# Performance work log

Measured on AMD Instinct MI355X. Metric: run time of the kernel, lower is better.

Reference implementation:

```python
import jax, jax.numpy as jnp
import numpy as np

DIM = 128      # input node feature dim
GS = 64        # SAGEConv output dim
AF = 32        # additional (ir_score) feature dim
NB = 2         # nb_classes
G = 8192       # num_graphs in batch
NPG = 16       # nodes per graph
N = G * NPG    # total nodes = 131072
E = 2097152    # total edges (avg degree 16)


def setup_inputs() -> dict:
    key = jax.random.key(0)
    ks = jax.random.split(key, 10)

    def w(k, shape, fan_in):
        return jax.random.normal(k, shape, jnp.float32) / np.sqrt(fan_in)

    return {
        "x": jax.random.normal(ks[0], (N, DIM), jnp.float32),
        "edge_index": jax.random.randint(ks[1], (2, E), 0, N),
        "set_indices": jax.random.randint(ks[2], (G, 2), 0, NPG),
        "batch_ids": jnp.repeat(jnp.arange(G), NPG),  # sorted graph ids, PyG style
        "ir_score": jax.random.uniform(ks[3], (G, AF), jnp.float32),
        "W_l": w(ks[4], (DIM, GS), DIM),
        "b_l": jnp.zeros((GS,), jnp.float32),
        "W_r": w(ks[5], (DIM, GS), DIM),
        "W_ir": w(ks[6], (AF, 2 * GS), AF),
        "b_ir": jnp.zeros((2 * GS,), jnp.float32),
        "W1": w(ks[7], ((2 * GS) * (2 * GS), 200), (2 * GS) * (2 * GS)),
        "b1": jnp.zeros((200,), jnp.float32),
        "W2": w(ks[8], (200, NB), 200),
        "b2": jnp.zeros((NB,), jnp.float32),
    }


def reference(x, edge_index, set_indices, batch_ids, ir_score,
              W_l, b_l, W_r, W_ir, b_ir, W1, b1, W2, b2):
    n = x.shape[0]
    src, dst = edge_index[0], edge_index[1]

    # SAGEConv (mean aggregation): out = lin_l(mean_{j in N(i)} x_j) + lin_r(x_i)
    agg = jax.ops.segment_sum(x[src], dst, num_segments=n)           # [N, DIM]
    deg = jax.ops.segment_sum(jnp.ones((src.shape[0],), x.dtype), dst, num_segments=n)
    mean = agg / jnp.maximum(deg, 1.0)[:, None]
    h = jax.nn.relu(mean @ W_l + b_l + x @ W_r)                      # [N, GS]

    # per-graph node counts -> index bases (cumsum), then global pair indices
    g = set_indices.shape[0]
    num_nodes = jax.ops.segment_sum(jnp.ones((n,), jnp.float32), batch_ids, num_segments=g)
    csum = jnp.cumsum(num_nodes.astype(jnp.int64))
    index_bases = jnp.concatenate([jnp.zeros((1,), jnp.int64), csum[:-1]])
    sib = index_bases[:, None] + set_indices                         # [G, 2]

    pair = h[sib].reshape(g, 2 * GS)                                 # gather + flatten

    # fusion: relu(linear(ir_score)) then per-graph outer product
    S = jax.nn.relu(ir_score @ W_ir + b_ir)                          # [G, 2*GS]
    outer = jnp.einsum('gi,gj->gij', pair, S).reshape(g, -1)         # [G, (2GS)^2]

    # decode MLP
    z = jax.nn.relu(outer @ W1 + b1)                                 # [G, 200]
    logits = z @ W2 + b2                                             # [G, NB]
    return logits
```

## Files before the change

### kernel.cpp

```cpp
#include <hip/hip_runtime.h>

#define NN   131072
#define GG   8192
#define EE   2097152
#define KBIG 16384
#define NPAD 224
#define NSPLIT 8
#define NSEL  16384
#define SBUCK 256
#define SUBC  4
#define SCAPS 336
#define SCAPT (SUBC*SCAPS)

typedef _Float16 half_t;
typedef __attribute__((ext_vector_type(8))) _Float16 half8;
typedef __attribute__((ext_vector_type(4))) float floatx4;

__device__ inline floatx4 mfma16(half8 a, half8 b, floatx4 c) {
  return __builtin_amdgcn_mfma_f32_16x16x32_f16(a, b, c, 0, 0, 0);
}

__global__ void prep_w(const float* __restrict__ Wl, const float* __restrict__ Wr,
                       half_t* __restrict__ Wt) {
  int idx = blockIdx.x * blockDim.x + threadIdx.x;
  int n = idx >> 7, k = idx & 127;
  float v = (n < 64) ? Wl[k * 64 + n] : Wr[k * 64 + (n - 64)];
  Wt[n * 128 + k] = (half_t)v;
}
__global__ void prep_w1p(const float* __restrict__ W1, half_t* __restrict__ W1p) {
  int idx = blockIdx.x * blockDim.x + threadIdx.x;
  int lane = idx & 63;
  int t = idx >> 6;
  int nt = t % 14; t /= 14;
  int jj = t & 1;  t >>= 1;
  int i  = t & 15; t >>= 4;
  int ph = t & 1;  t >>= 1;
  int split = t;
  int n = nt * 16 + (lane & 15);
  int k0 = split * 2048 + i * 128 + ph * 64 + jj * 32 + (lane >> 4) * 8;
  half8 v;
#pragma unroll
  for (int e = 0; e < 8; e++)
    v[e] = (half_t)((n < 200) ? W1[(size_t)(k0 + e) * 200 + n] : 0.f);
  *(half8*)(W1p + (size_t)idx * 8) = v;
}

__global__ void set_slots(const int* __restrict__ set_idx, int* __restrict__ nodemap,
                          int* __restrict__ slot_node) {
  int idx = blockIdx.x * blockDim.x + threadIdx.x;
  int g = idx >> 1, which = idx & 1;
  int node = g * 16 + set_idx[g * 2 + which];
  slot_node[idx] = node;
  nodemap[node] = idx;
}

__global__ void filter_scatter(const int* __restrict__ src, const int* __restrict__ dst,
                               const int* __restrict__ nodemap,
                               int* __restrict__ scnt, unsigned int* __restrict__ sbuf) {
  int e = blockIdx.x * blockDim.x + threadIdx.x;
  int d = dst[e];
  int slot = nodemap[d];
  if (slot >= 0) {
    int b = slot >> 6;
    int sub = blockIdx.x & (SUBC - 1);
    int pos = atomicAdd(&scnt[(b * SUBC + sub) * 16], 1);
    if (pos < SCAPS)
      sbuf[(size_t)(b * SUBC + sub) * SCAPS + pos] =
          (unsigned int)src[e] | ((unsigned int)(slot & 63) << 17);
  }
}

__global__ __launch_bounds__(256) void y_gemm(const float* __restrict__ x,
                                              const half_t* __restrict__ WtG,
                                              half_t* __restrict__ y16) {
  __shared__ half_t wlds[64 * 128];
  __shared__ half_t ybuf[64 * 72];
  int tid = threadIdx.x, w = tid >> 6, lane = tid & 63;
  int m = lane & 15, q = lane >> 4, kc = q * 8;
#pragma unroll
  for (int it = 0; it < 4; it++) {
    int cb = (it * 4 + w) * 64;
    const half_t* g = WtG + ((size_t)cb + lane) * 8;
    half_t* l = wlds + (size_t)cb * 8;
    __builtin_amdgcn_global_load_lds((const __attribute__((address_space(1))) uint32_t*)g,
                                     (__attribute__((address_space(3))) uint32_t*)l, 16, 0, 0);
  }
  int node0 = blockIdx.x * 64 + w * 16;
  float4 xu[4][2];
#pragma unroll
  for (int step = 0; step < 4; step++) {
    const float* xp = x + (size_t)(node0 + m) * 128 + step * 32 + kc;
    xu[step][0] = *(const float4*)xp;
    xu[step][1] = *(const float4*)(xp + 4);
  }
  __syncthreads();
  floatx4 acc[4];
#pragma unroll
  for (int nt = 0; nt < 4; nt++) acc[nt] = (floatx4){0.f, 0.f, 0.f, 0.f};
#pragma unroll
  for (int step = 0; step < 4; step++) {
    float4 u0 = xu[step][0], u1 = xu[step][1];
    half8 av = {(half_t)u0.x, (half_t)u0.y, (half_t)u0.z, (half_t)u0.w,
                (half_t)u1.x, (half_t)u1.y, (half_t)u1.z, (half_t)u1.w};
    int k0 = step * 32 + kc;
#pragma unroll
    for (int nt = 0; nt < 4; nt++) {
      half8 bv = *(const half8*)(wlds + (nt * 16 + m) * 128 + k0);
      acc[nt] = mfma16(av, bv, acc[nt]);
    }
  }
#pragma unroll
  for (int nt = 0; nt < 4; nt++)
#pragma unroll
    for (int r = 0; r < 4; r++)
      ybuf[(w * 16 + q * 4 + r) * 72 + nt * 16 + m] = (half_t)acc[nt][r];
  __syncthreads();
#pragma unroll
  for (int c = tid; c < 512; c += 256) {
    int row = c >> 3, co = (c & 7) * 8;
    *(half8*)(y16 + (size_t)(blockIdx.x * 64 + row) * 64 + co) =
        *(const half8*)(ybuf + row * 72 + co);
  }
}

__global__ __launch_bounds__(256) void r_slots(const float* __restrict__ x,
                                               const half_t* __restrict__ WtG,
                                               const float* __restrict__ b_l,
                                               const int* __restrict__ slot_node,
                                               half_t* __restrict__ r_slot) {
  int tid = threadIdx.x, w = tid >> 6, lane = tid & 63;
  int m = lane & 15, q = lane >> 4, kc = q * 8;
  int s0 = blockIdx.x * 64 + w * 16;
  int node = slot_node[s0 + m];
  floatx4 acc[4];
#pragma unroll
  for (int nt = 0; nt < 4; nt++) acc[nt] = (floatx4){0.f, 0.f, 0.f, 0.f};
#pragma unroll
  for (int step = 0; step < 4; step++) {
    int k0 = step * 32 + kc;
    const float* xp = x + (size_t)node * 128 + k0;
    float4 u0 = *(const float4*)xp;
    float4 u1 = *(const float4*)(xp + 4);
    half8 av = {(half_t)u0.x, (half_t)u0.y, (half_t)u0.z, (half_t)u0.w,
                (half_t)u1.x, (half_t)u1.y, (half_t)u1.z, (half_t)u1.w};
#pragma unroll
    for (int nt = 0; nt < 4; nt++) {
      half8 bv = *(const half8*)(WtG + (size_t)(64 + nt * 16 + m) * 128 + k0);
      acc[nt] = mfma16(av, bv, acc[nt]);
    }
  }
#pragma unroll
  for (int nt = 0; nt < 4; nt++) {
    int n = nt * 16 + m;
    float bias = b_l[n];
#pragma unroll
    for (int r = 0; r < 4; r++) {
      int s = s0 + q * 4 + r;
      r_slot[(size_t)s * 64 + n] = (half_t)(acc[nt][r] + bias);
    }
  }
}

__global__ __launch_bounds__(256) void slot_agg(const unsigned int* __restrict__ sbuf,
                                                const int* __restrict__ scnt,
                                                const half_t* __restrict__ y16,
                                                const half_t* __restrict__ r_slot,
                                                half_t* __restrict__ h_slot) {
  __shared__ int sorted[SCAPT];
  __shared__ int hist[64];
  __shared__ int base[64];
  __shared__ int start[65];
  int b = blockIdx.x, tid = threadIdx.x;
  if (tid < 64) hist[tid] = 0;
  __syncthreads();
  unsigned int myedge[2 * SUBC];
  int mycnt = 0;
#pragma unroll
  for (int sub = 0; sub < SUBC; sub++) {
    int n = scnt[(b * SUBC + sub) * 16]; if (n > SCAPS) n = SCAPS;
    const unsigned int* eb = sbuf + (size_t)(b * SUBC + sub) * SCAPS;
    for (int e = tid; e < n; e += 256) {
      unsigned int pk = eb[e];
      myedge[mycnt++] = pk;
      atomicAdd(&hist[pk >> 17], 1);
    }
  }
  __syncthreads();
  if (tid < 64) {
    int v = hist[tid];
    int sum = v;
#pragma unroll
    for (int off = 1; off < 64; off <<= 1) {
      int u = __shfl_up(sum, off);
      if (tid >= off) sum += u;
    }
    start[tid] = sum - v;
    base[tid]  = sum - v;
    if (tid == 63) start[64] = sum;
  }
  __syncthreads();
  for (int i = 0; i < mycnt; i++) {
    unsigned int pk = myedge[i];
    int pos = atomicAdd(&base[pk >> 17], 1);
    sorted[pos] = (int)(pk & 0x1FFFF);
  }
  __syncthreads();
  int s = tid >> 2, p = tid & 3;
  int e0 = start[s], e1 = start[s + 1];
  float acc[16];
#pragma unroll
  for (int j = 0; j < 16; j++) acc[j] = 0.f;
  int e = e0;
  for (; e + 2 <= e1; e += 2) {
    int s0 = sorted[e], s1 = sorted[e + 1];
    const half8* p0 = (const half8*)(y16 + (size_t)s0 * 64 + p * 16);
    const half8* p1 = (const half8*)(y16 + (size_t)s1 * 64 + p * 16);
    half8 a0 = p0[0], c0 = p0[1], a1 = p1[0], c1 = p1[1];
#pragma unroll
    for (int j = 0; j < 8; j++) {
      acc[j]     += (float)a0[j] + (float)a1[j];
      acc[8 + j] += (float)c0[j] + (float)c1[j];
    }
  }
  if (e < e1) {
    int s0 = sorted[e];
    const half8* p0 = (const half8*)(y16 + (size_t)s0 * 64 + p * 16);
    half8 a0 = p0[0], c0 = p0[1];
#pragma unroll
    for (int j = 0; j < 8; j++) { acc[j] += (float)a0[j]; acc[8 + j] += (float)c0[j]; }
  }
  int slot = b * 64 + s;
  float inv = 1.0f / fmaxf((float)(e1 - e0), 1.0f);
  const half8* rr = (const half8*)(r_slot + (size_t)slot * 64 + p * 16);
  half8 r0 = rr[0], r1 = rr[1];
  half8 o0, o1;
#pragma unroll
  for (int j = 0; j < 8; j++) {
    o0[j] = (half_t)fmaxf(acc[j] * inv + (float)r0[j], 0.f);
    o1[j] = (half_t)fmaxf(acc[8 + j] * inv + (float)r1[j], 0.f);
  }
  half8* hp = (half8*)(h_slot + (size_t)slot * 64 + p * 16);
  hp[0] = o0;
  hp[1] = o1;
}

__global__ void s_pair_kernel(const float* __restrict__ ir, const float* __restrict__ W_ir,
                              const float* __restrict__ b_ir, half_t* __restrict__ S16,
                              const half_t* __restrict__ h_slot,
                              const int* __restrict__ nodemap,
                              const int* __restrict__ set_idx, half_t* __restrict__ pair16) {
  int idx = blockIdx.x * blockDim.x + threadIdx.x;
  int g = idx >> 7, o = idx & 127;
  const float* irow = ir + g * 32;
  float sv = b_ir[o];
#pragma unroll
  for (int a = 0; a < 32; a++) sv += irow[a] * W_ir[a * 128 + o];
  S16[idx] = (half_t)fmaxf(sv, 0.f);
  int which = o >> 6, c = o & 63;
  int node = g * 16 + set_idx[g * 2 + which];
  int slot = nodemap[node];
  pair16[idx] = h_slot[(size_t)slot * 64 + c];
}

__global__ __launch_bounds__(256, 2) void biggemm(const half_t* __restrict__ pair16,
                                                  const half_t* __restrict__ S16,
                                                  const half_t* __restrict__ W1p,
                                                  float* __restrict__ zpart) {
  __shared__ __align__(16) half_t bbuf[2][28 * 512];
  __shared__ half_t pls[16][128];
  int bx = blockIdx.x;
  int mt = bx >> 3, split = bx & 7;
  int g0 = mt * 128;
  int tid = threadIdx.x, w = tid >> 6, lane = tid & 63;
  int wm = w >> 1, wn = w & 1;
  int m = lane & 15, q = lane >> 4, kc = q * 8;
  int ntb = wn * 7;

  auto stage = [&](int ph, int ii, int buf) {
#pragma unroll
    for (int ff = 0; ff < 7; ff++) {
      int f = ff * 4 + w;
      const half_t* gsrc = W1p + ((((size_t)(split * 2 + ph) * 16 + ii) * 28) + f) * 512 + lane * 8;
      half_t* ldst = &bbuf[buf][f * 512];
      __builtin_amdgcn_global_load_lds((const __attribute__((address_space(1))) uint32_t*)gsrc,
                                       (__attribute__((address_space(3))) uint32_t*)ldst, 16, 0, 0);
    }
  };

  stage(0, 0, 0);

  {
    int row = tid & 127, sel = tid >> 7;
    half8 pa = *(const half8*)(pair16 + (size_t)(g0 + row) * 128 + split * 16 + sel * 8);
#pragma unroll
    for (int j = 0; j < 8; j++) pls[sel * 8 + j][row] = pa[j];
  }

  floatx4 acc[4][7];
#pragma unroll
  for (int sb = 0; sb < 4; sb++)
#pragma unroll
    for (int t = 0; t < 7; t++) acc[sb][t] = (floatx4){0.f, 0.f, 0.f, 0.f};

  half8 sf[4][2];
#pragma unroll
  for (int ph = 0; ph < 2; ph++) {
#pragma unroll
    for (int sub = 0; sub < 4; sub++) {
      int grow = g0 + wm * 64 + sub * 16 + m;
#pragma unroll
      for (int j2 = 0; j2 < 2; j2++)
        sf[sub][j2] = *(const half8*)(S16 + (size_t)grow * 128 + ph * 64 + j2 * 32 + kc);
    }
#pragma unroll
    for (int i = 0; i < 16; i++) {
      int s = ph * 16 + i;
      int cur = s & 1;
      __syncthreads();
      half_t p0 = pls[i][wm * 64 + 0 * 16 + m];
      half_t p1 = pls[i][wm * 64 + 1 * 16 + m];
      half_t p2 = pls[i][wm * 64 + 2 * 16 + m];
      half_t p3 = pls[i][wm * 64 + 3 * 16 + m];
      if (s < 31) {
        int s1 = s + 1;
        stage(s1 >> 4, s1 & 15, cur ^ 1);
      }
      const half_t* bb = bbuf[cur];
#pragma unroll
      for (int jj = 0; jj < 2; jj++) {
        half8 a0 = sf[0][jj] * p0;
        half8 a1 = sf[1][jj] * p1;
        half8 a2 = sf[2][jj] * p2;
        half8 a3 = sf[3][jj] * p3;
#pragma unroll
        for (int t = 0; t < 7; t++) {
          half8 bv = *(const half8*)(bb + (jj * 14 + ntb + t) * 512 + lane * 8);
          acc[0][t] = mfma16(a0, bv, acc[0][t]);
          acc[1][t] = mfma16(a1, bv, acc[1][t]);
          acc[2][t] = mfma16(a2, bv, acc[2][t]);
          acc[3][t] = mfma16(a3, bv, acc[3][t]);
        }
      }
    }
  }

#pragma unroll
  for (int sub = 0; sub < 4; sub++)
#pragma unroll
    for (int t = 0; t < 7; t++)
#pragma unroll
      for (int r = 0; r < 4; r++) {
        int row = g0 + wm * 64 + sub * 16 + q * 4 + r;
        zpart[((size_t)split * GG + row) * NPAD + (ntb + t) * 16 + m] = acc[sub][t][r];
      }
}

__global__ __launch_bounds__(256) void reduce_mlp(const float* __restrict__ zpart,
                                                  const float* __restrict__ b1,
                                                  const float* __restrict__ W2,
                                                  const float* __restrict__ b2,
                                                  float* __restrict__ out) {
  int tid = threadIdx.x;
  int w = tid >> 6, lane = tid & 63;
  int g = blockIdx.x * 4 + w;
  float p0 = 0.f, p1 = 0.f;
#pragma unroll
  for (int qq = 0; qq < 4; qq++) {
    int c = qq * 64 + lane;
    if (c < 200) {
      float z = 0.f;
#pragma unroll
      for (int sp = 0; sp < NSPLIT; sp++)
        z += zpart[((size_t)sp * GG + g) * NPAD + c];
      z += b1[c];
      z = fmaxf(z, 0.f);
      p0 += z * W2[c * 2];
      p1 += z * W2[c * 2 + 1];
    }
  }
#pragma unroll
  for (int off = 32; off; off >>= 1) {
    p0 += __shfl_down(p0, off);
    p1 += __shfl_down(p1, off);
  }
  if (lane == 0) {
    out[g * 2] = p0 + b2[0];
    out[g * 2 + 1] = p1 + b2[1];
  }
}

extern "C" void kernel_launch(void* const* d_in, const int* in_sizes, int n_in,
                              void* d_out, int out_size, void* d_ws, size_t ws_size,
                              hipStream_t stream) {
  const float* x     = (const float*)d_in[0];
  const int*   ei    = (const int*)d_in[1];
  const int*   setix = (const int*)d_in[2];
  const float* ir    = (const float*)d_in[4];
  const float* W_l   = (const float*)d_in[5];
  const float* b_l   = (const float*)d_in[6];
  const float* W_r   = (const float*)d_in[7];
  const float* W_ir  = (const float*)d_in[8];
  const float* b_ir  = (const float*)d_in[9];
  const float* W1    = (const float*)d_in[10];
  const float* b1    = (const float*)d_in[11];
  const float* W2    = (const float*)d_in[12];
  const float* b2    = (const float*)d_in[13];
  float* out = (float*)d_out;

  char* ws = (char*)d_ws;
  size_t off = 0;
  auto alloc = [&](size_t bytes) -> void* {
    void* p = ws + off;
    off = (off + bytes + 255) & ~(size_t)255;
    return p;
  };
  size_t pool_start = off;
  int* nodemap   = (int*)alloc((size_t)NN * 4);
  int* slot_node = (int*)alloc((size_t)NSEL * 4);
  int* scnt      = (int*)alloc((size_t)SBUCK * SUBC * 16 * 4);
  unsigned int* sbuf = (unsigned int*)alloc((size_t)SBUCK * SUBC * SCAPS * 4);
  half_t* y16    = (half_t*)alloc((size_t)NN * 64 * 2);
  half_t* r_slot = (half_t*)alloc((size_t)NSEL * 64 * 2);
  half_t* h_slot = (half_t*)alloc((size_t)NSEL * 64 * 2);
  float* zpart = (float*)(ws + pool_start);
  {
    size_t zend = pool_start + (((size_t)NSPLIT * GG * NPAD * 4 + 255) & ~(size_t)255);
    if (off < zend) off = zend;
  }
  half_t* Wt     = (half_t*)alloc(128 * 128 * 2);
  half_t* W1p    = (half_t*)alloc((size_t)NPAD * KBIG * 2);
  half_t* S16    = (half_t*)alloc((size_t)GG * 128 * 2);
  half_t* pair16 = (half_t*)alloc((size_t)GG * 128 * 2);
  (void)ws_size; (void)in_sizes; (void)n_in; (void)out_size;

  const int* esrc = ei;
  const int* edst = ei + EE;

  hipMemsetAsync(nodemap, 0xFF, (size_t)NN * 4, stream);
  hipMemsetAsync(scnt, 0, (size_t)SBUCK * SUBC * 16 * 4, stream);

  prep_w<<<(128 * 128) / 256, 256, 0, stream>>>(W_l, W_r, Wt);
  prep_w1p<<<(NPAD * KBIG / 8) / 256, 256, 0, stream>>>(W1, W1p);

  set_slots<<<NSEL / 256, 256, 0, stream>>>(setix, nodemap, slot_node);
  filter_scatter<<<EE / 256, 256, 0, stream>>>(esrc, edst, nodemap, scnt, sbuf);

  y_gemm<<<NN / 64, 256, 0, stream>>>(x, Wt, y16);
  r_slots<<<NSEL / 64, 256, 0, stream>>>(x, Wt, b_l, slot_node, r_slot);
  slot_agg<<<SBUCK, 256, 0, stream>>>(sbuf, scnt, y16, r_slot, h_slot);

  s_pair_kernel<<<(GG * 128) / 256, 256, 0, stream>>>(ir, W_ir, b_ir, S16, h_slot, nodemap, setix, pair16);

  biggemm<<<(GG / 128) * NSPLIT, 256, 0, stream>>>(pair16, S16, W1p, zpart);
  reduce_mlp<<<GG / 4, 256, 0, stream>>>(zpart, b1, W2, b2, out);
}
```

Before: 260.2 us.

## Load W1 tiles directly into registers instead of LDS double-buffering in biggemm

Measured after the change: 329.9 us. 26.8% more time.

```diff
diff --git a/kernel.cpp b/kernel.cpp
--- a/kernel.cpp
+++ b/kernel.cpp
@@ -266,7 +266,6 @@
                                                   const half_t* __restrict__ S16,
                                                   const half_t* __restrict__ W1p,
                                                   float* __restrict__ zpart) {
-  __shared__ __align__(16) half_t bbuf[2][28 * 512];
   __shared__ half_t pls[16][128];
   int bx = blockIdx.x;
   int mt = bx >> 3, split = bx & 7;
@@ -276,31 +275,27 @@
   int m = lane & 15, q = lane >> 4, kc = q * 8;
   int ntb = wn * 7;
 
-  auto stage = [&](int ph, int ii, int buf) {
-#pragma unroll
-    for (int ff = 0; ff < 7; ff++) {
-      int f = ff * 4 + w;
-      const half_t* gsrc = W1p + ((((size_t)(split * 2 + ph) * 16 + ii) * 28) + f) * 512 + lane * 8;
-      half_t* ldst = &bbuf[buf][f * 512];
-      __builtin_amdgcn_global_load_lds((const __attribute__((address_space(1))) uint32_t*)gsrc,
-                                       (__attribute__((address_space(3))) uint32_t*)ldst, 16, 0, 0);
-    }
-  };
-
-  stage(0, 0, 0);
-
   {
     int row = tid & 127, sel = tid >> 7;
     half8 pa = *(const half8*)(pair16 + (size_t)(g0 + row) * 128 + split * 16 + sel * 8);
 #pragma unroll
     for (int j = 0; j < 8; j++) pls[sel * 8 + j][row] = pa[j];
   }
+  __syncthreads();
 
   floatx4 acc[4][7];
 #pragma unroll
   for (int sb = 0; sb < 4; sb++)
 #pragma unroll
     for (int t = 0; t < 7; t++) acc[sb][t] = (floatx4){0.f, 0.f, 0.f, 0.f};
+
+  const half_t* bp = W1p + ((size_t)split * 64 * 14 + ntb) * 512 + lane * 8;
+  const size_t USTRIDE = 14 * 512;
+
+  half8 pbA[7], pbB[7];
+#pragma unroll
+  for (int t = 0; t < 7; t++) pbA[t] = *(const half8*)(bp + t * 512);
+  bp += USTRIDE;
 
   half8 sf[4][2];
 #pragma unroll
@@ -314,31 +309,43 @@
     }
 #pragma unroll
     for (int i = 0; i < 16; i++) {
-      int s = ph * 16 + i;
-      int cur = s & 1;
-      __syncthreads();
+      const int s = ph * 16 + i;
       half_t p0 = pls[i][wm * 64 + 0 * 16 + m];
       half_t p1 = pls[i][wm * 64 + 1 * 16 + m];
       half_t p2 = pls[i][wm * 64 + 2 * 16 + m];
       half_t p3 = pls[i][wm * 64 + 3 * 16 + m];
+#pragma unroll
+      for (int t = 0; t < 7; t++) pbB[t] = *(const half8*)(bp + t * 512);
+      bp += USTRIDE;
+      {
+        half8 a0 = sf[0][0] * p0;
+        half8 a1 = sf[1][0] * p1;
+        half8 a2 = sf[2][0] * p2;
+        half8 a3 = sf[3][0] * p3;
+#pragma unroll
+        for (int t = 0; t < 7; t++) {
+          acc[0][t] = mfma16(a0, pbA[t], acc[0][t]);
+          acc[1][t] = mfma16(a1, pbA[t], acc[1][t]);
+          acc[2][t] = mfma16(a2, pbA[t], acc[2][t]);
+          acc[3][t] = mfma16(a3, pbA[t], acc[3][t]);
+        }
+      }
       if (s < 31) {
-        int s1 = s + 1;
-        stage(s1 >> 4, s1 & 15, cur ^ 1);
+#pragma unroll
+        for (int t = 0; t < 7; t++) pbA[t] = *(const half8*)(bp + t * 512);
+        bp += USTRIDE;
       }
-      const half_t* bb = bbuf[cur];
-#pragma unroll
-      for (int jj = 0; jj < 2; jj++) {
-        half8 a0 = sf[0][jj] * p0;
-        half8 a1 = sf[1][jj] * p1;
-        half8 a2 = sf[2][jj] * p2;
-        half8 a3 = sf[3][jj] * p3;
+      {
+        half8 a0 = sf[0][1] * p0;
+        half8 a1 = sf[1][1] * p1;
+        half8 a2 = sf[2][1] * p2;
+        half8 a3 = sf[3][1] * p3;
 #pragma unroll
         for (int t = 0; t < 7; t++) {
-          half8 bv = *(const half8*)(bb + (jj * 14 + ntb + t) * 512 + lane * 8);
-          acc[0][t] = mfma16(a0, bv, acc[0][t]);
-          acc[1][t] = mfma16(a1, bv, acc[1][t]);
-          acc[2][t] = mfma16(a2, bv, acc[2][t]);
-          acc[3][t] = mfma16(a3, bv, acc[3][t]);
+          acc[0][t] = mfma16(a0, pbB[t], acc[0][t]);
+          acc[1][t] = mfma16(a1, pbB[t], acc[1][t]);
+          acc[2][t] = mfma16(a2, pbB[t], acc[2][t]);
+          acc[3][t] = mfma16(a3, pbB[t], acc[3][t]);
         }
       }
     }
```
